# Optimization experiments

Measured on AMD Instinct MI355X. Metric: run time of the kernel, lower is better.

The kernel has to match this reference:

```python
import jax, jax.numpy as jnp
import numpy as np

N_STARS = 100000
N_ZERNIKES = 45
BATCH = 2048


def setup_inputs() -> dict:
    key = jax.random.key(0)
    k1, k2, k3 = jax.random.split(key, 3)
    # Observed star positions (unique enough in float32 random draws)
    obs_pos = jax.random.normal(k1, (N_STARS, 2), dtype=jnp.float32) * 1000.0
    # Prior Zernike coefficients per observed star
    zks_prior = jax.random.normal(k2, (N_STARS, N_ZERNIKES), dtype=jnp.float32)
    # Query positions are exact rows of obs_pos (the layer does exact-match search)
    sel = jax.random.randint(k3, (BATCH,), 0, N_STARS)
    positions = obs_pos[sel]
    return {"positions": positions, "obs_pos": obs_pos, "zks_prior": zks_prior}


def reference(positions, obs_pos, zks_prior):
    # Faithful to tf.where(tf.equal(obs_pos, pos))[0, 0]:
    # tf.equal broadcasts (n_stars, 2) == (2,) elementwise; tf.where lists True
    # coords in row-major order; [0, 0] is the row index of the FIRST True
    # element anywhere (x OR y coordinate match). We replicate that exactly by
    # flattening the (n_stars, 2) comparison and taking argmax // 2.
    eq = obs_pos[None, :, :] == positions[:, None, :]          # (B, N, 2) bool
    flat = eq.reshape(eq.shape[0], -1)                          # (B, 2N)
    indices = jnp.argmax(flat, axis=1) // 2                     # first-match row
    batch_zks = zks_prior[indices]                              # (B, n_zernikes)
    return batch_zks[:, :, None, None]                          # (B, n_zernikes, 1, 1)
```

## Files before the change

kernel.cpp:

```cpp
#include <hip/hip_runtime.h>
#include <cstdint>


#define LOG2_TABLE 18
#define TABLE_SIZE (1u << LOG2_TABLE)
#define TABLE_MASK (TABLE_SIZE - 1u)
#define EMPTY64    0xFFFFFFFFFFFFFFFFull
#define NO_IDX     0xFFFFFFFFu

typedef unsigned long long u64;

__device__ __forceinline__ uint32_t hmix(uint32_t x) {
    x ^= x >> 16; x *= 0x7feb352du;
    x ^= x >> 15; x *= 0x846ca68bu;
    x ^= x >> 16;
    return x;
}

__device__ __forceinline__ void ht_insert(u64* __restrict__ tab,
                                          uint32_t kb, uint32_t idx) {
    u64 pack = ((u64)kb << 32) | (u64)idx;
    uint32_t h = hmix(kb) & TABLE_MASK;
    for (;;) {
        u64 cur = tab[h];
        if ((uint32_t)(cur >> 32) == kb) {
            atomicMin(&tab[h], pack);
            return;
        }
        if (cur == EMPTY64) {
            u64 old = atomicCAS(&tab[h], EMPTY64, pack);
            if (old == EMPTY64) return;
            if ((uint32_t)(old >> 32) == kb) { atomicMin(&tab[h], pack); return; }
        }
        h = (h + 1u) & TABLE_MASK;
    }
}

__device__ __forceinline__ uint32_t ht_lookup(const u64* __restrict__ tab,
                                              uint32_t kb) {
    uint32_t h = hmix(kb) & TABLE_MASK;
    for (;;) {
        u64 cur = tab[h];
        if ((uint32_t)(cur >> 32) == kb) return (uint32_t)cur;
        if (cur == EMPTY64) return NO_IDX;
        h = (h + 1u) & TABLE_MASK;
    }
}

__global__ void clear_kernel(ulonglong2* __restrict__ ws, int n16) {
    int t = blockIdx.x * blockDim.x + threadIdx.x;
    if (t < n16) ws[t] = make_ulonglong2(EMPTY64, EMPTY64);
}

__global__ void build_kernel(const float2* __restrict__ obs,
                             u64* __restrict__ ws, int n_stars) {
    int i = blockIdx.x * blockDim.x + threadIdx.x;
    if (i >= n_stars) return;
    u64* tx = ws;
    u64* ty = ws + TABLE_SIZE;
    float2 s = obs[i];
    ht_insert(tx, __float_as_uint(s.x), (uint32_t)i);
    ht_insert(ty, __float_as_uint(s.y), (uint32_t)i);
}

__global__ void probe_gather_kernel(const float2* __restrict__ qpos,
                                    const float* __restrict__ zks,
                                    const u64* __restrict__ ws,
                                    float* __restrict__ out,
                                    int batch, int n_zk) {
    int gid  = blockIdx.x * blockDim.x + threadIdx.x;
    int wid  = gid >> 6;
    int lane = gid & 63;
    if (wid >= batch) return;

    const u64* tx = ws;
    const u64* ty = ws + TABLE_SIZE;

    float2 q = qpos[wid];
    uint32_t ix = ht_lookup(tx, __float_as_uint(q.x));
    uint32_t iy = ht_lookup(ty, __float_as_uint(q.y));
    uint32_t idx = ix < iy ? ix : iy;
    if (idx == NO_IDX) idx = 0;

    if (lane < n_zk)
        out[(long long)wid * n_zk + lane] = zks[(long long)idx * n_zk + lane];
}

#define SBLOCK 256
#define QCHUNK 512
#define SENTINEL 0x7fffffff

__global__ void init_idx(int* __restrict__ minidx, int batch) {
    int t = blockIdx.x * blockDim.x + threadIdx.x;
    if (t < batch) minidx[t] = SENTINEL;
}

__global__ __launch_bounds__(SBLOCK)
void scan_kernel(const float2* __restrict__ obs,
                 const float2* __restrict__ qpos,
                 int* __restrict__ minidx,
                 int n_stars, int batch) {
    __shared__ float2 q[QCHUNK];
    const int qbase = blockIdx.y * QCHUNK;
    for (int j = threadIdx.x; j < QCHUNK; j += SBLOCK) {
        int qi = qbase + j;
        if (qi < batch) q[j] = qpos[qi];
        else { float nv = __int_as_float(0x7fc00000); q[j] = make_float2(nv, nv); }
    }
    __syncthreads();
    const int i = blockIdx.x * SBLOCK + threadIdx.x;
    float sx, sy;
    if (i < n_stars) { float2 s = obs[i]; sx = s.x; sy = s.y; }
    else { sx = __int_as_float(0x7fc00000); sy = sx; }
    #pragma unroll 8
    for (int j = 0; j < QCHUNK; ++j) {
        float2 Q = q[j];
        if (sx == Q.x || sy == Q.y) atomicMin(&minidx[qbase + j], i);
    }
}

__global__ void gather_kernel(const float* __restrict__ zks,
                              const int* __restrict__ minidx,
                              float* __restrict__ out,
                              int batch, int n_zk) {
    int t = blockIdx.x * blockDim.x + threadIdx.x;
    int total = batch * n_zk;
    if (t >= total) return;
    int b = t / n_zk;
    int k = t - b * n_zk;
    int idx = minidx[b];
    if (idx == SENTINEL) idx = 0;
    out[t] = zks[(long long)idx * n_zk + k];
}

extern "C" void kernel_launch(void* const* d_in, const int* in_sizes, int n_in,
                              void* d_out, int out_size, void* d_ws, size_t ws_size,
                              hipStream_t stream) {
    const float2* qpos = (const float2*)d_in[0];
    const float2* obs  = (const float2*)d_in[1];
    const float*  zks  = (const float*)d_in[2];

    const int batch   = in_sizes[0] / 2;
    const int n_stars = in_sizes[1] / 2;
    const int n_zk    = in_sizes[2] / n_stars;

    float* out = (float*)d_out;

    const size_t table_bytes = (size_t)2 * TABLE_SIZE * sizeof(u64);

    if (ws_size >= table_bytes) {
        u64* ws = (u64*)d_ws;
        int n16 = (int)(table_bytes / 16);
        clear_kernel<<<(n16 + 255) / 256, 256, 0, stream>>>((ulonglong2*)ws, n16);
        build_kernel<<<(n_stars + 255) / 256, 256, 0, stream>>>(obs, ws, n_stars);
        int threads = batch * 64;
        probe_gather_kernel<<<(threads + 255) / 256, 256, 0, stream>>>(
            qpos, zks, ws, out, batch, n_zk);
    } else {
        int* minidx = (int*)d_ws;
        init_idx<<<(batch + 255) / 256, 256, 0, stream>>>(minidx, batch);
        dim3 grid((n_stars + SBLOCK - 1) / SBLOCK, (batch + QCHUNK - 1) / QCHUNK);
        scan_kernel<<<grid, SBLOCK, 0, stream>>>(obs, qpos, minidx, n_stars, batch);
        int total = batch * n_zk;
        gather_kernel<<<(total + 255) / 256, 256, 0, stream>>>(zks, minidx, out,
                                                               batch, n_zk);
    }
}
```

Baseline: 39.40 us.

## Fuse clear, build and probe into one cooperative kernel with grid syncs

```diff
diff --git a/kernel.cpp b/kernel.cpp
--- a/kernel.cpp
+++ b/kernel.cpp
@@ -1,5 +1,8 @@
 #include <hip/hip_runtime.h>
+#include <hip/hip_cooperative_groups.h>
 #include <cstdint>
+
+namespace cg = cooperative_groups;
 
 
 #define LOG2_TABLE 18
@@ -47,6 +50,47 @@
     }
 }
 
+__global__ __launch_bounds__(256)
+void fused_kernel(const float2* __restrict__ qpos,
+                  const float2* __restrict__ obs,
+                  const float* __restrict__ zks,
+                  float* __restrict__ out,
+                  u64* __restrict__ ws,
+                  int n_stars, int batch, int n_zk) {
+    cg::grid_group grid = cg::this_grid();
+    const int tid      = blockIdx.x * blockDim.x + threadIdx.x;
+    const int nthreads = gridDim.x * blockDim.x;
+
+    ulonglong2* w2 = (ulonglong2*)ws;
+    for (uint32_t t = tid; t < TABLE_SIZE; t += nthreads)
+        w2[t] = make_ulonglong2(EMPTY64, EMPTY64);
+
+    grid.sync();
+
+    u64* tx = ws;
+    u64* ty = ws + TABLE_SIZE;
+    for (int i = tid; i < n_stars; i += nthreads) {
+        float2 s = obs[i];
+        ht_insert(tx, __float_as_uint(s.x), (uint32_t)i);
+        ht_insert(ty, __float_as_uint(s.y), (uint32_t)i);
+    }
+
+    grid.sync();
+
+    const int wid    = tid >> 6;
+    const int lane   = tid & 63;
+    const int nwaves = nthreads >> 6;
+    for (int q = wid; q < batch; q += nwaves) {
+        float2 Q = qpos[q];
+        uint32_t ix = ht_lookup(tx, __float_as_uint(Q.x));
+        uint32_t iy = ht_lookup(ty, __float_as_uint(Q.y));
+        uint32_t idx = ix < iy ? ix : iy;
+        if (idx == NO_IDX) idx = 0;
+        if (lane < n_zk)
+            out[(long long)q * n_zk + lane] = zks[(long long)idx * n_zk + lane];
+    }
+}
+
 __global__ void clear_kernel(ulonglong2* __restrict__ ws, int n16) {
     int t = blockIdx.x * blockDim.x + threadIdx.x;
     if (t < n16) ws[t] = make_ulonglong2(EMPTY64, EMPTY64);
@@ -56,11 +100,9 @@
                              u64* __restrict__ ws, int n_stars) {
     int i = blockIdx.x * blockDim.x + threadIdx.x;
     if (i >= n_stars) return;
-    u64* tx = ws;
-    u64* ty = ws + TABLE_SIZE;
     float2 s = obs[i];
-    ht_insert(tx, __float_as_uint(s.x), (uint32_t)i);
-    ht_insert(ty, __float_as_uint(s.y), (uint32_t)i);
+    ht_insert(ws, __float_as_uint(s.x), (uint32_t)i);
+    ht_insert(ws + TABLE_SIZE, __float_as_uint(s.y), (uint32_t)i);
 }
 
 __global__ void probe_gather_kernel(const float2* __restrict__ qpos,
@@ -72,16 +114,11 @@
     int wid  = gid >> 6;
     int lane = gid & 63;
     if (wid >= batch) return;
-
-    const u64* tx = ws;
-    const u64* ty = ws + TABLE_SIZE;
-
     float2 q = qpos[wid];
-    uint32_t ix = ht_lookup(tx, __float_as_uint(q.x));
-    uint32_t iy = ht_lookup(ty, __float_as_uint(q.y));
+    uint32_t ix = ht_lookup(ws, __float_as_uint(q.x));
+    uint32_t iy = ht_lookup(ws + TABLE_SIZE, __float_as_uint(q.y));
     uint32_t idx = ix < iy ? ix : iy;
     if (idx == NO_IDX) idx = 0;
-
     if (lane < n_zk)
         out[(long long)wid * n_zk + lane] = zks[(long long)idx * n_zk + lane];
 }
@@ -140,9 +177,9 @@
     const float2* obs  = (const float2*)d_in[1];
     const float*  zks  = (const float*)d_in[2];
 
-    const int batch   = in_sizes[0] / 2;
-    const int n_stars = in_sizes[1] / 2;
-    const int n_zk    = in_sizes[2] / n_stars;
+    int batch   = in_sizes[0] / 2;
+    int n_stars = in_sizes[1] / 2;
+    int n_zk    = in_sizes[2] / n_stars;
 
     float* out = (float*)d_out;
 
@@ -150,12 +187,21 @@
 
     if (ws_size >= table_bytes) {
         u64* ws = (u64*)d_ws;
-        int n16 = (int)(table_bytes / 16);
-        clear_kernel<<<(n16 + 255) / 256, 256, 0, stream>>>((ulonglong2*)ws, n16);
-        build_kernel<<<(n_stars + 255) / 256, 256, 0, stream>>>(obs, ws, n_stars);
-        int threads = batch * 64;
-        probe_gather_kernel<<<(threads + 255) / 256, 256, 0, stream>>>(
-            qpos, zks, ws, out, batch, n_zk);
+
+        void* args[] = { (void*)&qpos, (void*)&obs, (void*)&zks,
+                         (void*)&out, (void*)&ws,
+                         (void*)&n_stars, (void*)&batch, (void*)&n_zk };
+        hipError_t err = hipLaunchCooperativeKernel(
+            (const void*)fused_kernel, dim3(512), dim3(256), args, 0, stream);
+
+        if (err != hipSuccess) {
+            int n16 = (int)(table_bytes / 16);
+            clear_kernel<<<(n16 + 255) / 256, 256, 0, stream>>>((ulonglong2*)ws, n16);
+            build_kernel<<<(n_stars + 255) / 256, 256, 0, stream>>>(obs, ws, n_stars);
+            int threads = batch * 64;
+            probe_gather_kernel<<<(threads + 255) / 256, 256, 0, stream>>>(
+                qpos, zks, ws, out, batch, n_zk);
+        }
     } else {
         int* minidx = (int*)d_ws;
         init_idx<<<(batch + 255) / 256, 256, 0, stream>>>(minidx, batch);
```

Measured after the change: 134.2 us. +240.7%, slower.
